# Kernel optimization log

Hardware: AMD Instinct MI355X
Metric: run time of the kernel (lower is better)

## Reference

```python
import jax, jax.numpy as jnp
import numpy as np

NUM_EXPERTS = 64
TOP_K = 8
NUM_TOKENS = 8192
HIDDEN = 1024
INTER = 512


def setup_inputs() -> dict:
    key = jax.random.key(0)
    k1, k2, k3, k4 = jax.random.split(key, 4)
    # 0.02 scale keeps activations in a sane range (randn weights with fan-in 1024)
    return {
        "hidden_states": jax.random.normal(k1, (NUM_TOKENS, HIDDEN), jnp.float32),
        "router_weight": jax.random.normal(k2, (HIDDEN, NUM_EXPERTS), jnp.float32) * 0.02,
        "merged_gate_up_proj": jax.random.normal(k3, (NUM_EXPERTS, HIDDEN, 2 * INTER), jnp.float32) * 0.02,
        "merged_down_proj": jax.random.normal(k4, (NUM_EXPERTS, INTER, HIDDEN), jnp.float32) * 0.02,
    }


def reference(hidden_states, router_weight, merged_gate_up_proj, merged_down_proj):
    T, H = hidden_states.shape
    E = router_weight.shape[1]

    # ---- Router: softmax over experts, top-k, renormalize top-k weights ----
    logits = hidden_states @ router_weight                       # [T, E]
    probs = jax.nn.softmax(logits, axis=-1)
    routing_weights, routing_indices = jax.lax.top_k(probs, TOP_K)  # [T, k]
    routing_weights = routing_weights / routing_weights.sum(-1, keepdims=True)

    # ---- Permute (haojun_permute_topk): replicate tokens topk times, stable-sort by expert ----
    flat_indices = routing_indices.reshape(-1)                   # [T*k]
    sort_order = jnp.argsort(flat_indices)                       # stable sort
    flat_states = jnp.repeat(hidden_states, TOP_K, axis=0)       # [T*k, H]
    permuted = flat_states[sort_order]                           # tokens grouped by expert
    group_sizes = jnp.bincount(flat_indices, length=E).astype(jnp.int32)  # tokens per expert

    # ---- Grouped MLP (grouped_gemm.gmm equivalent): y_i = x_i @ W[expert(i)] ----
    merged = jax.lax.ragged_dot(permuted, merged_gate_up_proj, group_sizes)  # [T*k, 2*I]
    gate, up = jnp.split(merged, 2, axis=-1)
    h = jax.nn.silu(gate) * up                                   # SiLU-gated (hidden_act='silu')
    expert_out = jax.lax.ragged_dot(h, merged_down_proj, group_sizes)        # [T*k, H]

    # ---- Unpermute: invert the sort, weight by routing probs, sum over top-k ----
    inv = jnp.argsort(sort_order)                                # unsort_order
    unpermuted = expert_out[inv].reshape(T, TOP_K, H)
    return (unpermuted * routing_weights[..., None]).sum(axis=1)  # [T, H]
```

## Files before the change

kernel.cpp:

```cpp
#include <hip/hip_runtime.h>
#include <cstdint>
#include <cstddef>

typedef __bf16 bf16_t;
typedef __bf16 bf16x8 __attribute__((ext_vector_type(8)));
typedef __bf16 bf16x4 __attribute__((ext_vector_type(4)));
typedef float f32x4 __attribute__((ext_vector_type(4)));

#define T_TOKENS 8192
#define HID 1024
#define INTER 512
#define NEXP 64
#define TOPK 8
#define NROWS (T_TOKENS * TOPK)
#define RT_TOK 16

typedef const unsigned int __attribute__((address_space(1)))* gptr_t;
typedef unsigned int __attribute__((address_space(3)))* lptr_t;

__device__ __forceinline__ void gload_lds16(const void* g, void* l) {
  __builtin_amdgcn_global_load_lds((gptr_t)g, (lptr_t)l, 16, 0, 0);
}

__device__ __forceinline__ f32x4 mfma16(bf16x8 a, bf16x8 b, f32x4 c) {
  return __builtin_amdgcn_mfma_f32_16x16x32_bf16(a, b, c, 0, 0, 0);
}

__device__ __forceinline__ int xcd_swizzle(int bid, int nwg) {
  int q = nwg >> 3;
  int xcd = bid & 7, i = bid >> 3;
  return xcd * q + i;
}

__global__ void transpose_cvt2_kernel(const float* __restrict__ w1, bf16_t* __restrict__ Wt1,
                                      const float* __restrict__ w2, bf16_t* __restrict__ Wt2,
                                      int* __restrict__ cntz) {
  const int tid = threadIdx.x;
  if (blockIdx.x == 0 && blockIdx.y == 0 && blockIdx.z == 0 && tid < 128) cntz[tid] = 0;

  const int e = blockIdx.z;
  const float* W; bf16_t* Wt; int K, k0;
  if (blockIdx.y < 16) {
    W = w1; Wt = Wt1; K = 1024; k0 = blockIdx.y * 64;
  } else {
    W = w2; Wt = Wt2; K = 512; k0 = (blockIdx.y - 16) * 64;
  }
  const int N = 1024;
  const int n0 = blockIdx.x * 64;

  __shared__ __align__(8) bf16_t tile[64][68];
  {
    const int r = tid >> 2, cq = tid & 3;
    const float* src = W + ((size_t)e * K + k0 + r) * N + n0 + cq * 16;
#pragma unroll
    for (int q = 0; q < 4; ++q) {
      float4 v = *(const float4*)(src + q * 4);
      bf16x4 b;
      b[0] = (bf16_t)v.x; b[1] = (bf16_t)v.y; b[2] = (bf16_t)v.z; b[3] = (bf16_t)v.w;
      *(bf16x4*)&tile[r][cq * 16 + q * 4] = b;
    }
  }
  __syncthreads();
  {
    const int nl = tid >> 2, kq = tid & 3;
    __align__(16) bf16_t tmp[16];
#pragma unroll
    for (int i = 0; i < 16; ++i) tmp[i] = tile[kq * 16 + i][nl];
    bf16_t* dst = Wt + ((size_t)e * N + n0 + nl) * K + k0 + kq * 16;
    *(bf16x8*)(dst + 0) = *(const bf16x8*)(tmp + 0);
    *(bf16x8*)(dst + 8) = *(const bf16x8*)(tmp + 8);
  }
}

__launch_bounds__(256, 2)
__global__ void router_kernel(const float* __restrict__ hs, const float* __restrict__ rw,
                              float* __restrict__ wval, int* __restrict__ widx,
                              bf16_t* __restrict__ hb, int* __restrict__ cnt) {
  const int t0 = blockIdx.x * RT_TOK;
  const int tid = threadIdx.x;
  const int lane = tid & 63, w = tid >> 6;
  __shared__ float hsl[RT_TOK][HID / 4][4];
  __shared__ float part[4][RT_TOK][NEXP];
  __shared__ int bh[NEXP];
  if (tid < NEXP) bh[tid] = 0;

  for (int i = tid; i < RT_TOK * (HID / 4); i += 256) {
    int t = i >> 8, c = i & 255;
    float4 v = ((const float4*)(hs + (size_t)(t0 + t) * HID))[c];
    *(float4*)&hsl[t][c][0] = v;
    bf16x4 o;
    o[0] = (bf16_t)v.x; o[1] = (bf16_t)v.y; o[2] = (bf16_t)v.z; o[3] = (bf16_t)v.w;
    *(bf16x4*)(hb + (size_t)(t0 + t) * HID + c * 4) = o;
  }
  __syncthreads();

  float acc[RT_TOK];
#pragma unroll
  for (int t = 0; t < RT_TOK; ++t) acc[t] = 0.f;
  const int kb = w * 256;
  for (int kc = 0; kc < 64; ++kc) {
    const int k = kb + kc * 4;
    float r0 = rw[(size_t)(k + 0) * NEXP + lane];
    float r1 = rw[(size_t)(k + 1) * NEXP + lane];
    float r2 = rw[(size_t)(k + 2) * NEXP + lane];
    float r3 = rw[(size_t)(k + 3) * NEXP + lane];
#pragma unroll
    for (int t = 0; t < RT_TOK; ++t) {
      float4 hv = *(const float4*)&hsl[t][(kb >> 2) + kc][0];
      acc[t] = fmaf(hv.x, r0, acc[t]);
      acc[t] = fmaf(hv.y, r1, acc[t]);
      acc[t] = fmaf(hv.z, r2, acc[t]);
      acc[t] = fmaf(hv.w, r3, acc[t]);
    }
  }
#pragma unroll
  for (int t = 0; t < RT_TOK; ++t) part[w][t][lane] = acc[t];
  __syncthreads();

  for (int j = 0; j < 4; ++j) {
    const int t = w * 4 + j;
    float logit = part[0][t][lane] + part[1][t][lane] + part[2][t][lane] + part[3][t][lane];
    float m = logit;
    for (int off = 32; off; off >>= 1) m = fmaxf(m, __shfl_xor(m, off));
    float ex = expf(logit - m);
    float Z = ex;
    for (int off = 32; off; off >>= 1) Z += __shfl_xor(Z, off);
    float p = ex / Z;
    float sum8 = 0.f;
    float outv[8]; int outi[8];
#pragma unroll
    for (int s = 0; s < 8; ++s) {
      float v = p; int idx = lane;
      for (int off = 32; off; off >>= 1) {
        float vv = __shfl_xor(v, off);
        int ii = __shfl_xor(idx, off);
        if (vv > v || (vv == v && ii < idx)) { v = vv; idx = ii; }
      }
      outv[s] = v; outi[s] = idx; sum8 += v;
      if (lane == idx) p = -1.f;
    }
    if (lane == 0) {
      float inv = 1.f / sum8;
#pragma unroll
      for (int s = 0; s < 8; ++s) {
        wval[(size_t)(t0 + t) * TOPK + s] = outv[s] * inv;
        widx[(size_t)(t0 + t) * TOPK + s] = outi[s];
        atomicAdd(&bh[outi[s]], 1);
      }
    }
  }
  __syncthreads();
  if (tid < NEXP) atomicAdd(&cnt[tid], bh[tid]);
}

__global__ void assign_kernel(const int* __restrict__ widx, const int* __restrict__ cnt,
                              int* __restrict__ cnt2, int* __restrict__ row_org,
                              int* __restrict__ seg) {
  __shared__ int segl[NEXP];
  const int tid = threadIdx.x;
  if (tid < NEXP) {
    int a = 0;
    for (int j = 0; j < tid; ++j) a += cnt[j];
    segl[tid] = a;
    if (blockIdx.x == 0) {
      seg[tid] = a;
      if (tid == NEXP - 1) seg[NEXP] = a + cnt[NEXP - 1];
    }
  }
  __syncthreads();
  for (int i = blockIdx.x * blockDim.x + tid; i < NROWS; i += gridDim.x * blockDim.x) {
    int e = widx[i];
    int p = segl[e] + atomicAdd(&cnt2[e], 1);
    row_org[p] = i;
  }
}

__launch_bounds__(256, 2)
__global__ void gemm1_kernel(const bf16_t* __restrict__ hb, const bf16_t* __restrict__ Wt1,
                             const int* __restrict__ row_org, const int* __restrict__ seg,
                             bf16_t* __restrict__ h) {
  const int bid = blockIdx.x + gridDim.x * (blockIdx.y + gridDim.y * blockIdx.z);
  const int swz = xcd_swizzle(bid, 16 * 4 * NEXP);
  const int mt = swz & 15;
  const int nt = (swz >> 4) & 3;
  const int e = swz >> 6;

  const int ms = seg[e];
  const int sz = seg[e + 1] - ms;
  const int n0 = nt * 128;
  const int tid = threadIdx.x;
  const int lane = tid & 63;
  const int wid = tid >> 6;
  const int wm = wid >> 1, wn = wid & 1;
  __shared__ __align__(16) bf16_t As[128 * 64];
  __shared__ __align__(16) bf16_t Bs[256 * 64];

  const int srow = tid >> 3;
  const int cg = (tid & 7) ^ (srow & 7);

  size_t boff[8];
#pragma unroll
  for (int b = 0; b < 8; ++b) {
    int brow = b * 32 + srow;
    int n = (brow < 128) ? (n0 + brow) : (512 + n0 + (brow - 128));
    boff[b] = ((size_t)e * 1024 + n) * 1024 + cg * 8;
  }
  const int l15 = lane & 15, l4 = lane >> 4;

  for (int m0 = mt * 128; m0 < sz; m0 += 16 * 128) {
    size_t aoff[4];
#pragma unroll
    for (int a = 0; a < 4; ++a) {
      int row = a * 32 + srow;
      int idx = m0 + row; if (idx >= sz) idx = sz - 1;
      aoff[a] = (size_t)(row_org[ms + idx] >> 3) * HID + cg * 8;
    }
    f32x4 accg[4][4], accu[4][4];
#pragma unroll
    for (int mi = 0; mi < 4; ++mi)
#pragma unroll
      for (int ni = 0; ni < 4; ++ni) {
        accg[mi][ni] = (f32x4){0.f, 0.f, 0.f, 0.f};
        accu[mi][ni] = (f32x4){0.f, 0.f, 0.f, 0.f};
      }

    for (int kt = 0; kt < 16; ++kt) {
      const int ko = kt * 64;
      __syncthreads();
#pragma unroll
      for (int a = 0; a < 4; ++a)
        gload_lds16(hb + aoff[a] + ko, (char*)As + a * 4096 + tid * 16);
#pragma unroll
      for (int b = 0; b < 8; ++b)
        gload_lds16(Wt1 + boff[b] + ko, (char*)Bs + b * 4096 + tid * 16);
      __syncthreads();
#pragma unroll
      for (int kf = 0; kf < 2; ++kf) {
        const int ch = kf * 4 + l4;
        bf16x8 af[4], bg[4], bu[4];
#pragma unroll
        for (int mi = 0; mi < 4; ++mi) {
          int r = wm * 64 + mi * 16 + l15;
          af[mi] = *(const bf16x8*)((const char*)As + r * 128 + ((ch ^ (r & 7)) << 4));
        }
#pragma unroll
        for (int ni = 0; ni < 4; ++ni) {
          int rg = wn * 64 + ni * 16 + l15;
          bg[ni] = *(const bf16x8*)((const char*)Bs + rg * 128 + ((ch ^ (rg & 7)) << 4));
          int ru = rg + 128;
          bu[ni] = *(const bf16x8*)((const char*)Bs + ru * 128 + ((ch ^ (ru & 7)) << 4));
        }
#pragma unroll
        for (int mi = 0; mi < 4; ++mi)
#pragma unroll
          for (int ni = 0; ni < 4; ++ni) {
            accg[mi][ni] = mfma16(af[mi], bg[ni], accg[mi][ni]);
            accu[mi][ni] = mfma16(af[mi], bu[ni], accu[mi][ni]);
          }
      }
    }
#pragma unroll
    for (int mi = 0; mi < 4; ++mi) {
#pragma unroll
      for (int j = 0; j < 4; ++j) {
        int mrow = wm * 64 + mi * 16 + l4 * 4 + j;
        int idx = m0 + mrow;
        if (idx < sz) {
          bf16_t* hrow = h + (size_t)(ms + idx) * INTER + n0 + wn * 64 + l15;
#pragma unroll
          for (int ni = 0; ni < 4; ++ni) {
            float g = accg[mi][ni][j];
            float u = accu[mi][ni][j];
            float s = g / (1.f + __expf(-g));
            hrow[ni * 16] = (bf16_t)(s * u);
          }
        }
      }
    }
  }
}

__launch_bounds__(256, 2)
__global__ void gemm2_kernel(const bf16_t* __restrict__ h, const bf16_t* __restrict__ Wt2,
                             const int* __restrict__ row_org, const int* __restrict__ seg,
                             bf16_t* __restrict__ eo) {
  const int bid = blockIdx.x + gridDim.x * (blockIdx.y + gridDim.y * blockIdx.z);
  const int swz = xcd_swizzle(bid, 16 * 8 * NEXP);
  const int mt = swz & 15;
  const int nt = (swz >> 4) & 7;
  const int e = swz >> 7;

  const int ms = seg[e];
  const int sz = seg[e + 1] - ms;
  const int n0 = nt * 128;
  const int tid = threadIdx.x;
  const int lane = tid & 63;
  const int wid = tid >> 6;
  const int wm = wid >> 1, wn = wid & 1;
  __shared__ __align__(16) bf16_t As[128 * 64];
  __shared__ __align__(16) bf16_t Bs[128 * 64];
  const int srow = tid >> 3;
  const int cg = (tid & 7) ^ (srow & 7);
  size_t boff[4];
#pragma unroll
  for (int b = 0; b < 4; ++b) {
    int brow = b * 32 + srow;
    boff[b] = ((size_t)e * 1024 + n0 + brow) * INTER + cg * 8;
  }
  const int l15 = lane & 15, l4 = lane >> 4;

  for (int m0 = mt * 128; m0 < sz; m0 += 16 * 128) {
    size_t aoff[4];
#pragma unroll
    for (int a = 0; a < 4; ++a) {
      int row = a * 32 + srow;
      int idx = m0 + row; if (idx >= sz) idx = sz - 1;
      aoff[a] = (size_t)(ms + idx) * INTER + cg * 8;
    }
    f32x4 acc[4][4];
#pragma unroll
    for (int mi = 0; mi < 4; ++mi)
#pragma unroll
      for (int ni = 0; ni < 4; ++ni) acc[mi][ni] = (f32x4){0.f, 0.f, 0.f, 0.f};

    for (int kt = 0; kt < 8; ++kt) {
      const int ko = kt * 64;
      __syncthreads();
#pragma unroll
      for (int a = 0; a < 4; ++a)
        gload_lds16(h + aoff[a] + ko, (char*)As + a * 4096 + tid * 16);
#pragma unroll
      for (int b = 0; b < 4; ++b)
        gload_lds16(Wt2 + boff[b] + ko, (char*)Bs + b * 4096 + tid * 16);
      __syncthreads();
#pragma unroll
      for (int kf = 0; kf < 2; ++kf) {
        const int ch = kf * 4 + l4;
        bf16x8 af[4], bb[4];
#pragma unroll
        for (int mi = 0; mi < 4; ++mi) {
          int r = wm * 64 + mi * 16 + l15;
          af[mi] = *(const bf16x8*)((const char*)As + r * 128 + ((ch ^ (r & 7)) << 4));
        }
#pragma unroll
        for (int ni = 0; ni < 4; ++ni) {
          int r = wn * 64 + ni * 16 + l15;
          bb[ni] = *(const bf16x8*)((const char*)Bs + r * 128 + ((ch ^ (r & 7)) << 4));
        }
#pragma unroll
        for (int mi = 0; mi < 4; ++mi)
#pragma unroll
          for (int ni = 0; ni < 4; ++ni)
            acc[mi][ni] = mfma16(af[mi], bb[ni], acc[mi][ni]);
      }
    }
#pragma unroll
    for (int mi = 0; mi < 4; ++mi) {
#pragma unroll
      for (int j = 0; j < 4; ++j) {
        int mrow = wm * 64 + mi * 16 + l4 * 4 + j;
        int idx = m0 + mrow;
        if (idx < sz) {
          int org = row_org[ms + idx];
          bf16_t* orow = eo + (size_t)org * HID + n0 + wn * 64 + l15;
#pragma unroll
          for (int ni = 0; ni < 4; ++ni)
            orow[ni * 16] = (bf16_t)acc[mi][ni][j];
        }
      }
    }
  }
}

__global__ void unpermute_kernel(const bf16_t* __restrict__ eo, const float* __restrict__ wval,
                                 float* __restrict__ out) {
  const int t = blockIdx.x * 2 + (threadIdx.x >> 7);
  const int c0 = (threadIdx.x & 127) * 8;
  float w[8];
#pragma unroll
  for (int s = 0; s < 8; ++s) w[s] = wval[(size_t)t * 8 + s];
  float acc[8] = {0.f, 0.f, 0.f, 0.f, 0.f, 0.f, 0.f, 0.f};
#pragma unroll
  for (int s = 0; s < 8; ++s) {
    bf16x8 v = *(const bf16x8*)(eo + ((size_t)t * 8 + s) * HID + c0);
#pragma unroll
    for (int q = 0; q < 8; ++q) acc[q] = fmaf(w[s], (float)v[q], acc[q]);
  }
  *(float4*)(out + (size_t)t * HID + c0) = *(float4*)&acc[0];
  *(float4*)(out + (size_t)t * HID + c0 + 4) = *(float4*)&acc[4];
}

extern "C" void kernel_launch(void* const* d_in, const int* in_sizes, int n_in,
                              void* d_out, int out_size, void* d_ws, size_t ws_size,
                              hipStream_t stream) {
  (void)in_sizes; (void)n_in; (void)ws_size; (void)out_size;
  const float* hs = (const float*)d_in[0];
  const float* rw = (const float*)d_in[1];
  const float* w1 = (const float*)d_in[2];
  const float* w2 = (const float*)d_in[3];
  float* out = (float*)d_out;

  char* p = (char*)d_ws;
  size_t off = 0;
  auto carve = [&](size_t bytes) {
    void* r = p + off;
    off = (off + bytes + 255) & ~(size_t)255;
    return r;
  };
  bf16_t* Wt1  = (bf16_t*)carve((size_t)NEXP * 1024 * 1024 * 2);
  bf16_t* Wt2  = (bf16_t*)carve((size_t)NEXP * 1024 * 512 * 2);
  bf16_t* hb   = (bf16_t*)carve((size_t)T_TOKENS * HID * 2);
  bf16_t* hmid = (bf16_t*)carve((size_t)NROWS * INTER * 2);
  float* wval  = (float*)carve((size_t)NROWS * 4);
  int* widx    = (int*)carve((size_t)NROWS * 4);
  int* row_org = (int*)carve((size_t)NROWS * 4);
  int* cnt     = (int*)carve(512);
  int* seg     = (int*)carve(66 * 4);
  int* cnt2    = cnt + 64;

  bf16_t* eo = Wt1;

  transpose_cvt2_kernel<<<dim3(16, 24, 64), 256, 0, stream>>>(w1, Wt1, w2, Wt2, cnt);
  router_kernel<<<T_TOKENS / RT_TOK, 256, 0, stream>>>(hs, rw, wval, widx, hb, cnt);
  assign_kernel<<<128, 256, 0, stream>>>(widx, cnt, cnt2, row_org, seg);
  gemm1_kernel<<<dim3(16, 4, NEXP), 256, 0, stream>>>(hb, Wt1, row_org, seg, hmid);
  gemm2_kernel<<<dim3(16, 8, NEXP), 256, 0, stream>>>(hmid, Wt2, row_org, seg, eo);
  unpermute_kernel<<<T_TOKENS / 2, 256, 0, stream>>>(eo, wval, out);
}
```

Baseline: 641.4 us.

## Double-buffer gemm1 with 512-thread 256-row tiles and overlapped prefetch

Rewrites the gate/up grouped GEMM to use 512-thread blocks with 256x(128 gate+128 up) tiles and double-buffered LDS. The next K slice is prefetched via global_load_lds while MFMAs run on the current buffer, with setprio around the MFMA bursts. The intent is to hide global-load latency and raise reuse per tile. In exchange it uses 128KB of LDS per block, which lowers occupancy, and makes the last partial tile of each expert coarser. Separately, the router drops its shared-memory histogram and issues global atomics directly per top-k choice.

Result: slower. 959.8 us (+49.6%).

```diff
diff --git a/kernel.cpp b/kernel.cpp
--- a/kernel.cpp
+++ b/kernel.cpp
@@ -81,8 +81,6 @@
   const int lane = tid & 63, w = tid >> 6;
   __shared__ float hsl[RT_TOK][HID / 4][4];
   __shared__ float part[4][RT_TOK][NEXP];
-  __shared__ int bh[NEXP];
-  if (tid < NEXP) bh[tid] = 0;
 
   for (int i = tid; i < RT_TOK * (HID / 4); i += 256) {
     int t = i >> 8, c = i & 255;
@@ -145,12 +143,10 @@
       for (int s = 0; s < 8; ++s) {
         wval[(size_t)(t0 + t) * TOPK + s] = outv[s] * inv;
         widx[(size_t)(t0 + t) * TOPK + s] = outi[s];
-        atomicAdd(&bh[outi[s]], 1);
-      }
-    }
-  }
-  __syncthreads();
-  if (tid < NEXP) atomicAdd(&cnt[tid], bh[tid]);
+        atomicAdd(&cnt[outi[s]], 1);
+      }
+    }
+  }
 }
 
 __global__ void assign_kernel(const int* __restrict__ widx, const int* __restrict__ cnt,
@@ -175,15 +171,15 @@
   }
 }
 
-__launch_bounds__(256, 2)
+__launch_bounds__(512, 2)
 __global__ void gemm1_kernel(const bf16_t* __restrict__ hb, const bf16_t* __restrict__ Wt1,
                              const int* __restrict__ row_org, const int* __restrict__ seg,
                              bf16_t* __restrict__ h) {
   const int bid = blockIdx.x + gridDim.x * (blockIdx.y + gridDim.y * blockIdx.z);
-  const int swz = xcd_swizzle(bid, 16 * 4 * NEXP);
-  const int mt = swz & 15;
-  const int nt = (swz >> 4) & 3;
-  const int e = swz >> 6;
+  const int swz = xcd_swizzle(bid, 8 * 4 * NEXP);
+  const int mt = swz & 7;
+  const int nt = (swz >> 3) & 3;
+  const int e = swz >> 5;
 
   const int ms = seg[e];
   const int sz = seg[e + 1] - ms;
@@ -191,88 +187,124 @@
   const int tid = threadIdx.x;
   const int lane = tid & 63;
   const int wid = tid >> 6;
-  const int wm = wid >> 1, wn = wid & 1;
-  __shared__ __align__(16) bf16_t As[128 * 64];
-  __shared__ __align__(16) bf16_t Bs[256 * 64];
+  const int wm = wid >> 2;
+  const int wn = wid & 3;
+
+  __shared__ __align__(16) bf16_t As[2][256 * 64];
+  __shared__ __align__(16) bf16_t Bs[2][256 * 64];
 
   const int srow = tid >> 3;
   const int cg = (tid & 7) ^ (srow & 7);
 
-  size_t boff[8];
-#pragma unroll
-  for (int b = 0; b < 8; ++b) {
-    int brow = b * 32 + srow;
+  size_t boff[4];
+#pragma unroll
+  for (int b = 0; b < 4; ++b) {
+    int brow = b * 64 + srow;
     int n = (brow < 128) ? (n0 + brow) : (512 + n0 + (brow - 128));
     boff[b] = ((size_t)e * 1024 + n) * 1024 + cg * 8;
   }
   const int l15 = lane & 15, l4 = lane >> 4;
 
-  for (int m0 = mt * 128; m0 < sz; m0 += 16 * 128) {
+  for (int m0 = mt * 256; m0 < sz; m0 += 8 * 256) {
     size_t aoff[4];
 #pragma unroll
     for (int a = 0; a < 4; ++a) {
-      int row = a * 32 + srow;
+      int row = a * 64 + srow;
       int idx = m0 + row; if (idx >= sz) idx = sz - 1;
       aoff[a] = (size_t)(row_org[ms + idx] >> 3) * HID + cg * 8;
     }
-    f32x4 accg[4][4], accu[4][4];
-#pragma unroll
-    for (int mi = 0; mi < 4; ++mi)
-#pragma unroll
-      for (int ni = 0; ni < 4; ++ni) {
-        accg[mi][ni] = (f32x4){0.f, 0.f, 0.f, 0.f};
-        accu[mi][ni] = (f32x4){0.f, 0.f, 0.f, 0.f};
-      }
+    f32x4 accg[8][2], accu[8][2];
+#pragma unroll
+    for (int mi = 0; mi < 8; ++mi)
+#pragma unroll
+      for (int gi = 0; gi < 2; ++gi) {
+        accg[mi][gi] = (f32x4){0.f, 0.f, 0.f, 0.f};
+        accu[mi][gi] = (f32x4){0.f, 0.f, 0.f, 0.f};
+      }
+
+#pragma unroll
+    for (int a = 0; a < 4; ++a)
+      gload_lds16(hb + aoff[a], (char*)&As[0][0] + a * 8192 + tid * 16);
+#pragma unroll
+    for (int a = 0; a < 4; ++a)
+      gload_lds16(Wt1 + boff[a], (char*)&Bs[0][0] + a * 8192 + tid * 16);
+    asm volatile("s_waitcnt vmcnt(0)\n\ts_barrier" ::: "memory");
 
     for (int kt = 0; kt < 16; ++kt) {
-      const int ko = kt * 64;
-      __syncthreads();
-#pragma unroll
-      for (int a = 0; a < 4; ++a)
-        gload_lds16(hb + aoff[a] + ko, (char*)As + a * 4096 + tid * 16);
-#pragma unroll
-      for (int b = 0; b < 8; ++b)
-        gload_lds16(Wt1 + boff[b] + ko, (char*)Bs + b * 4096 + tid * 16);
-      __syncthreads();
-#pragma unroll
-      for (int kf = 0; kf < 2; ++kf) {
-        const int ch = kf * 4 + l4;
-        bf16x8 af[4], bg[4], bu[4];
-#pragma unroll
-        for (int mi = 0; mi < 4; ++mi) {
-          int r = wm * 64 + mi * 16 + l15;
-          af[mi] = *(const bf16x8*)((const char*)As + r * 128 + ((ch ^ (r & 7)) << 4));
-        }
-#pragma unroll
-        for (int ni = 0; ni < 4; ++ni) {
-          int rg = wn * 64 + ni * 16 + l15;
-          bg[ni] = *(const bf16x8*)((const char*)Bs + rg * 128 + ((ch ^ (rg & 7)) << 4));
-          int ru = rg + 128;
-          bu[ni] = *(const bf16x8*)((const char*)Bs + ru * 128 + ((ch ^ (ru & 7)) << 4));
-        }
-#pragma unroll
-        for (int mi = 0; mi < 4; ++mi)
-#pragma unroll
-          for (int ni = 0; ni < 4; ++ni) {
-            accg[mi][ni] = mfma16(af[mi], bg[ni], accg[mi][ni]);
-            accu[mi][ni] = mfma16(af[mi], bu[ni], accu[mi][ni]);
+      const int b = kt & 1;
+      const char* Ab = (const char*)&As[b][0];
+      const char* Bb = (const char*)&Bs[b][0];
+      const bool pf = (kt + 1 < 16);
+      const int ko = (kt + 1) * 64;
+
+      bf16x8 bfr[8];
+#pragma unroll
+      for (int p = 0; p < 4; ++p) {
+        const int mi0 = p * 2;
+        if (p == 0) {
+#pragma unroll
+          for (int kf = 0; kf < 2; ++kf) {
+            const int ch = kf * 4 + l4;
+#pragma unroll
+            for (int gi = 0; gi < 2; ++gi) {
+              int rg = wn * 32 + gi * 16 + l15;
+              bfr[kf * 4 + gi] = *(const bf16x8*)(Bb + rg * 128 + ((ch ^ (rg & 7)) << 4));
+              int ru = rg + 128;
+              bfr[kf * 4 + 2 + gi] = *(const bf16x8*)(Bb + ru * 128 + ((ch ^ (ru & 7)) << 4));
+            }
           }
-      }
-    }
-#pragma unroll
-    for (int mi = 0; mi < 4; ++mi) {
+        }
+        bf16x8 af[4];
+#pragma unroll
+        for (int mi = 0; mi < 2; ++mi)
+#pragma unroll
+          for (int kf = 0; kf < 2; ++kf) {
+            int r = wm * 128 + (mi0 + mi) * 16 + l15;
+            int ch = kf * 4 + l4;
+            af[mi * 2 + kf] = *(const bf16x8*)(Ab + r * 128 + ((ch ^ (r & 7)) << 4));
+          }
+        if (pf && p == 0) {
+#pragma unroll
+          for (int a = 0; a < 4; ++a)
+            gload_lds16(hb + aoff[a] + ko, (char*)&As[b ^ 1][0] + a * 8192 + tid * 16);
+        }
+        if (pf && p == 1) {
+#pragma unroll
+          for (int a = 0; a < 4; ++a)
+            gload_lds16(Wt1 + boff[a] + ko, (char*)&Bs[b ^ 1][0] + a * 8192 + tid * 16);
+        }
+        __builtin_amdgcn_s_barrier();
+        __builtin_amdgcn_s_setprio(1);
+#pragma unroll
+        for (int mi = 0; mi < 2; ++mi)
+#pragma unroll
+          for (int kf = 0; kf < 2; ++kf)
+#pragma unroll
+            for (int gi = 0; gi < 2; ++gi) {
+              accg[mi0 + mi][gi] = mfma16(af[mi * 2 + kf], bfr[kf * 4 + gi], accg[mi0 + mi][gi]);
+              accu[mi0 + mi][gi] = mfma16(af[mi * 2 + kf], bfr[kf * 4 + 2 + gi], accu[mi0 + mi][gi]);
+            }
+        __builtin_amdgcn_s_setprio(0);
+        if (p == 3) {
+          asm volatile("s_waitcnt vmcnt(0)" ::: "memory");
+        }
+        __builtin_amdgcn_s_barrier();
+      }
+    }
+#pragma unroll
+    for (int mi = 0; mi < 8; ++mi) {
 #pragma unroll
       for (int j = 0; j < 4; ++j) {
-        int mrow = wm * 64 + mi * 16 + l4 * 4 + j;
+        int mrow = wm * 128 + mi * 16 + l4 * 4 + j;
         int idx = m0 + mrow;
         if (idx < sz) {
-          bf16_t* hrow = h + (size_t)(ms + idx) * INTER + n0 + wn * 64 + l15;
-#pragma unroll
-          for (int ni = 0; ni < 4; ++ni) {
-            float g = accg[mi][ni][j];
-            float u = accu[mi][ni][j];
+          bf16_t* hrow = h + (size_t)(ms + idx) * INTER + n0 + wn * 32 + l15;
+#pragma unroll
+          for (int gi = 0; gi < 2; ++gi) {
+            float g = accg[mi][gi][j];
+            float u = accu[mi][gi][j];
             float s = g / (1.f + __expf(-g));
-            hrow[ni * 16] = (bf16_t)(s * u);
+            hrow[gi * 16] = (bf16_t)(s * u);
           }
         }
       }
@@ -423,7 +455,7 @@
   transpose_cvt2_kernel<<<dim3(16, 24, 64), 256, 0, stream>>>(w1, Wt1, w2, Wt2, cnt);
   router_kernel<<<T_TOKENS / RT_TOK, 256, 0, stream>>>(hs, rw, wval, widx, hb, cnt);
   assign_kernel<<<128, 256, 0, stream>>>(widx, cnt, cnt2, row_org, seg);
-  gemm1_kernel<<<dim3(16, 4, NEXP), 256, 0, stream>>>(hb, Wt1, row_org, seg, hmid);
+  gemm1_kernel<<<dim3(8, 4, NEXP), 512, 0, stream>>>(hb, Wt1, row_org, seg, hmid);
   gemm2_kernel<<<dim3(16, 8, NEXP), 256, 0, stream>>>(hmid, Wt2, row_org, seg, eo);
   unpermute_kernel<<<T_TOKENS / 2, 256, 0, stream>>>(eo, wval, out);
 }
```

## Fuse weight transpose and router into one interleaved prep kernel

Applied to the files above, without the earlier changes.

Merges the weight transpose/convert kernel and the router kernel into a single launch. Router blocks are interleaved every 49th block among the transpose blocks, so the two kinds of work run concurrently and one launch boundary goes away. Global per-expert atomics are replaced with per-block count writes that assign_kernel reduces, which removes the need to zero the counters before the router runs. The cost is a larger shared-memory union and an extra reduction pass over 512 entries per expert in assign_kernel.

Result: no change. 635.7 us (-0.9%).

```diff
diff --git a/kernel.cpp b/kernel.cpp
--- a/kernel.cpp
+++ b/kernel.cpp
@@ -14,6 +14,9 @@
 #define TOPK 8
 #define NROWS (T_TOKENS * TOPK)
 #define RT_TOK 16
+#define NRBLK (T_TOKENS / RT_TOK)
+#define NTBLK (16 * 24 * 64)
+#define PREP_STRIDE 49
 
 typedef const unsigned int __attribute__((address_space(1)))* gptr_t;
 typedef unsigned int __attribute__((address_space(3)))* lptr_t;
@@ -32,62 +35,66 @@
   return xcd * q + i;
 }
 
-__global__ void transpose_cvt2_kernel(const float* __restrict__ w1, bf16_t* __restrict__ Wt1,
-                                      const float* __restrict__ w2, bf16_t* __restrict__ Wt2,
-                                      int* __restrict__ cntz) {
+union PrepSmem {
+  struct { float hsl[RT_TOK][HID / 4][4];
+           float part[4][RT_TOK][NEXP]; } r;
+  bf16_t tile[64][68];
+};
+
+__launch_bounds__(256, 2)
+__global__ void prep_kernel(const float* __restrict__ hs, const float* __restrict__ rw,
+                            float* __restrict__ wval, int* __restrict__ widx,
+                            bf16_t* __restrict__ hb, int* __restrict__ bcnt,
+                            int* __restrict__ cnt2,
+                            const float* __restrict__ w1, bf16_t* __restrict__ Wt1,
+                            const float* __restrict__ w2, bf16_t* __restrict__ Wt2) {
+  __shared__ PrepSmem sm;
   const int tid = threadIdx.x;
-  if (blockIdx.x == 0 && blockIdx.y == 0 && blockIdx.z == 0 && tid < 128) cntz[tid] = 0;
-
-  const int e = blockIdx.z;
-  const float* W; bf16_t* Wt; int K, k0;
-  if (blockIdx.y < 16) {
-    W = w1; Wt = Wt1; K = 1024; k0 = blockIdx.y * 64;
-  } else {
-    W = w2; Wt = Wt2; K = 512; k0 = (blockIdx.y - 16) * 64;
-  }
-  const int N = 1024;
-  const int n0 = blockIdx.x * 64;
-
-  __shared__ __align__(8) bf16_t tile[64][68];
-  {
-    const int r = tid >> 2, cq = tid & 3;
-    const float* src = W + ((size_t)e * K + k0 + r) * N + n0 + cq * 16;
-#pragma unroll
-    for (int q = 0; q < 4; ++q) {
-      float4 v = *(const float4*)(src + q * 4);
-      bf16x4 b;
-      b[0] = (bf16_t)v.x; b[1] = (bf16_t)v.y; b[2] = (bf16_t)v.z; b[3] = (bf16_t)v.w;
-      *(bf16x4*)&tile[r][cq * 16 + q * 4] = b;
-    }
-  }
-  __syncthreads();
-  {
-    const int nl = tid >> 2, kq = tid & 3;
-    __align__(16) bf16_t tmp[16];
-#pragma unroll
-    for (int i = 0; i < 16; ++i) tmp[i] = tile[kq * 16 + i][nl];
-    bf16_t* dst = Wt + ((size_t)e * N + n0 + nl) * K + k0 + kq * 16;
-    *(bf16x8*)(dst + 0) = *(const bf16x8*)(tmp + 0);
-    *(bf16x8*)(dst + 8) = *(const bf16x8*)(tmp + 8);
-  }
-}
-
-__launch_bounds__(256, 2)
-__global__ void router_kernel(const float* __restrict__ hs, const float* __restrict__ rw,
-                              float* __restrict__ wval, int* __restrict__ widx,
-                              bf16_t* __restrict__ hb, int* __restrict__ cnt) {
-  const int t0 = blockIdx.x * RT_TOK;
-  const int tid = threadIdx.x;
+  const int bid = blockIdx.x;
+
+  if (bid % PREP_STRIDE != 0) {
+    const int tb = bid - bid / PREP_STRIDE - 1;
+    const int e = tb / 384;
+    const int r384 = tb % 384;
+    const int ky = r384 >> 4, nt = r384 & 15;
+    const float* W; bf16_t* Wt; int K, k0;
+    if (ky < 16) { W = w1; Wt = Wt1; K = 1024; k0 = ky * 64; }
+    else         { W = w2; Wt = Wt2; K = 512;  k0 = (ky - 16) * 64; }
+    const int N = 1024;
+    const int n0 = nt * 64;
+    {
+      const int rr = tid >> 2, cq = tid & 3;
+      const float* src = W + ((size_t)e * K + k0 + rr) * N + n0 + cq * 16;
+#pragma unroll
+      for (int q = 0; q < 4; ++q) {
+        float4 v = *(const float4*)(src + q * 4);
+        bf16x4 b;
+        b[0] = (bf16_t)v.x; b[1] = (bf16_t)v.y; b[2] = (bf16_t)v.z; b[3] = (bf16_t)v.w;
+        *(bf16x4*)&sm.tile[rr][cq * 16 + q * 4] = b;
+      }
+    }
+    __syncthreads();
+    {
+      const int nl = tid >> 2, kq = tid & 3;
+      __align__(16) bf16_t tmp[16];
+#pragma unroll
+      for (int i = 0; i < 16; ++i) tmp[i] = sm.tile[kq * 16 + i][nl];
+      bf16_t* dst = Wt + ((size_t)e * N + n0 + nl) * K + k0 + kq * 16;
+      *(bf16x8*)(dst + 0) = *(const bf16x8*)(tmp + 0);
+      *(bf16x8*)(dst + 8) = *(const bf16x8*)(tmp + 8);
+    }
+    return;
+  }
+
+  const int rb = bid / PREP_STRIDE;
+  const int t0 = rb * RT_TOK;
   const int lane = tid & 63, w = tid >> 6;
-  __shared__ float hsl[RT_TOK][HID / 4][4];
-  __shared__ float part[4][RT_TOK][NEXP];
-  __shared__ int bh[NEXP];
-  if (tid < NEXP) bh[tid] = 0;
+  if (rb == 0 && tid < NEXP) cnt2[tid] = 0;
 
   for (int i = tid; i < RT_TOK * (HID / 4); i += 256) {
     int t = i >> 8, c = i & 255;
     float4 v = ((const float4*)(hs + (size_t)(t0 + t) * HID))[c];
-    *(float4*)&hsl[t][c][0] = v;
+    *(float4*)&sm.r.hsl[t][c][0] = v;
     bf16x4 o;
     o[0] = (bf16_t)v.x; o[1] = (bf16_t)v.y; o[2] = (bf16_t)v.z; o[3] = (bf16_t)v.w;
     *(bf16x4*)(hb + (size_t)(t0 + t) * HID + c * 4) = o;
@@ -106,7 +113,7 @@
     float r3 = rw[(size_t)(k + 3) * NEXP + lane];
 #pragma unroll
     for (int t = 0; t < RT_TOK; ++t) {
-      float4 hv = *(const float4*)&hsl[t][(kb >> 2) + kc][0];
+      float4 hv = *(const float4*)&sm.r.hsl[t][(kb >> 2) + kc][0];
       acc[t] = fmaf(hv.x, r0, acc[t]);
       acc[t] = fmaf(hv.y, r1, acc[t]);
       acc[t] = fmaf(hv.z, r2, acc[t]);
@@ -114,12 +121,17 @@
     }
   }
 #pragma unroll
-  for (int t = 0; t < RT_TOK; ++t) part[w][t][lane] = acc[t];
+  for (int t = 0; t < RT_TOK; ++t) sm.r.part[w][t][lane] = acc[t];
+  __syncthreads();
+
+  int* bh = (int*)&sm;
+  if (tid < NEXP) bh[tid] = 0;
   __syncthreads();
 
   for (int j = 0; j < 4; ++j) {
     const int t = w * 4 + j;
-    float logit = part[0][t][lane] + part[1][t][lane] + part[2][t][lane] + part[3][t][lane];
+    float logit = sm.r.part[0][t][lane] + sm.r.part[1][t][lane] +
+                  sm.r.part[2][t][lane] + sm.r.part[3][t][lane];
     float m = logit;
     for (int off = 32; off; off >>= 1) m = fmaxf(m, __shfl_xor(m, off));
     float ex = expf(logit - m);
@@ -150,21 +162,29 @@
     }
   }
   __syncthreads();
-  if (tid < NEXP) atomicAdd(&cnt[tid], bh[tid]);
-}
-
-__global__ void assign_kernel(const int* __restrict__ widx, const int* __restrict__ cnt,
+  if (tid < NEXP) bcnt[tid * NRBLK + rb] = bh[tid];
+}
+
+__global__ void assign_kernel(const int* __restrict__ widx, const int* __restrict__ bcnt,
                               int* __restrict__ cnt2, int* __restrict__ row_org,
                               int* __restrict__ seg) {
+  __shared__ int tot[NEXP];
   __shared__ int segl[NEXP];
   const int tid = threadIdx.x;
   if (tid < NEXP) {
+    const int4* src = (const int4*)(bcnt + (size_t)tid * NRBLK);
     int a = 0;
-    for (int j = 0; j < tid; ++j) a += cnt[j];
+    for (int j = 0; j < NRBLK / 4; ++j) { int4 v = src[j]; a += v.x + v.y + v.z + v.w; }
+    tot[tid] = a;
+  }
+  __syncthreads();
+  if (tid < NEXP) {
+    int a = 0;
+    for (int j = 0; j < tid; ++j) a += tot[j];
     segl[tid] = a;
     if (blockIdx.x == 0) {
       seg[tid] = a;
-      if (tid == NEXP - 1) seg[NEXP] = a + cnt[NEXP - 1];
+      if (tid == NEXP - 1) seg[NEXP] = a + tot[NEXP - 1];
     }
   }
   __syncthreads();
@@ -414,15 +434,15 @@
   float* wval  = (float*)carve((size_t)NROWS * 4);
   int* widx    = (int*)carve((size_t)NROWS * 4);
   int* row_org = (int*)carve((size_t)NROWS * 4);
-  int* cnt     = (int*)carve(512);
+  int* bcnt    = (int*)carve((size_t)NEXP * NRBLK * 4);
+  int* cnt2    = (int*)carve(256);
   int* seg     = (int*)carve(66 * 4);
-  int* cnt2    = cnt + 64;
 
   bf16_t* eo = Wt1;
 
-  transpose_cvt2_kernel<<<dim3(16, 24, 64), 256, 0, stream>>>(w1, Wt1, w2, Wt2, cnt);
-  router_kernel<<<T_TOKENS / RT_TOK, 256, 0, stream>>>(hs, rw, wval, widx, hb, cnt);
-  assign_kernel<<<128, 256, 0, stream>>>(widx, cnt, cnt2, row_org, seg);
+  prep_kernel<<<NRBLK + NTBLK, 256, 0, stream>>>(hs, rw, wval, widx, hb, bcnt, cnt2,
+                                                 w1, Wt1, w2, Wt2);
+  assign_kernel<<<128, 256, 0, stream>>>(widx, bcnt, cnt2, row_org, seg);
   gemm1_kernel<<<dim3(16, 4, NEXP), 256, 0, stream>>>(hb, Wt1, row_org, seg, hmid);
   gemm2_kernel<<<dim3(16, 8, NEXP), 256, 0, stream>>>(hmid, Wt2, row_org, seg, eo);
   unpermute_kernel<<<T_TOKENS / 2, 256, 0, stream>>>(eo, wval, out);
```
